# Optimization experiments

Measured on AMD Instinct MI355X. Metric: run time of the kernel, lower is better.

## Reference

```python
import jax, jax.numpy as jnp
import numpy as np

D_MODEL = 1024

def setup_inputs() -> dict:
    key = jax.random.key(0)
    kx, kq, kk, kv, ko = jax.random.split(key, 5)
    x = jax.random.normal(kx, (4, 4096, D_MODEL), dtype=jnp.float32)
    w_q = jax.random.normal(kq, (D_MODEL, D_MODEL), dtype=jnp.float32)
    w_k = jax.random.normal(kk, (D_MODEL, D_MODEL), dtype=jnp.float32)
    w_v = jax.random.normal(kv, (D_MODEL, D_MODEL), dtype=jnp.float32)
    w_o = jax.random.normal(ko, (D_MODEL, D_MODEL), dtype=jnp.float32)
    return {"x": x, "w_q": w_q, "w_k": w_k, "w_v": w_v, "w_o": w_o}

def reference(x, w_q, w_k, w_v, w_o):
    # Q/K/V projections: [B,T,D] @ [D,D] -> [B,T,D]
    q = jnp.einsum('btd,de->bte', x, w_q)
    k = jnp.einsum('btd,de->bte', x, w_k)
    v = jnp.einsum('btd,de->bte', x, w_v)
    # Unnormalized attention: scores [B,T,T] (no softmax)
    scores = jnp.einsum('btd,bsd->bts', q, k)
    attn_output = jnp.einsum('bts,bsd->btd', scores, v)
    # Output projection
    output = jnp.einsum('btd,de->bte', attn_output, w_o)
    return output
```

## Files before the change

kernel.cpp:

```cpp
#include <hip/hip_runtime.h>
#include <hip/hip_bf16.h>
#include <stdint.h>

typedef unsigned short u16;
typedef short bf16x8 __attribute__((ext_vector_type(8)));
typedef float f32x4 __attribute__((ext_vector_type(4)));

#define GLOAD16(gp, lp) __builtin_amdgcn_global_load_lds( \
    (const __attribute__((address_space(1))) uint32_t*)(gp), \
    (__attribute__((address_space(3))) uint32_t*)(lp), 16, 0, 0)

#define VMCNT10 do { asm volatile("s_waitcnt vmcnt(10)" ::: "memory"); \
                     __builtin_amdgcn_sched_barrier(0); } while (0)
#define SBAR    do { __builtin_amdgcn_s_barrier(); \
                     __builtin_amdgcn_sched_barrier(0); } while (0)
#define LGKM0   do { asm volatile("s_waitcnt lgkmcnt(0)" ::: "memory"); \
                     __builtin_amdgcn_sched_barrier(0); } while (0)

__device__ __forceinline__ u16 f2bf(float f) {
  union { float f; uint32_t u; } x; x.f = f;
  return (u16)((x.u + 0x7FFFu + ((x.u >> 16) & 1u)) >> 16);
}
__device__ __forceinline__ float bf2f(u16 h) {
  union { uint32_t u; float f; } x; x.u = (uint32_t)h << 16;
  return x.f;
}

__device__ __forceinline__ void xcd_swizzle(int& bx, int& by, int& bz) {
  const int gx = gridDim.x, gy = gridDim.y;
  const int nwg = gx * gy * (int)gridDim.z;
  const int lin = ((int)blockIdx.z * gy + (int)blockIdx.y) * gx + (int)blockIdx.x;
  const int q = nwg >> 3;
  const int wl = (lin & 7) * q + (lin >> 3);
  bz = wl / (gx * gy);
  const int rem = wl - bz * gx * gy;
  by = rem / gx;
  bx = rem - by * gx;
}

__global__ __launch_bounds__(256) void cast_all(const float* __restrict__ x,
                                                const float* __restrict__ wq,
                                                const float* __restrict__ wk,
                                                const float* __restrict__ wv,
                                                const float* __restrict__ wo,
                                                u16* __restrict__ xb,
                                                u16* __restrict__ xT,
                                                u16* __restrict__ WA,
                                                u16* __restrict__ WBb) {
  __shared__ float tile[64][65];
  const int lin = blockIdx.x;
  const int t = threadIdx.x;
  const int lr = t >> 2, lc = (t & 3) * 16;
  if (lin < 4096) {
    const int d0 = (lin & 15) * 64;
    const int t0 = (lin >> 4) * 64;
    const float* src = x + (size_t)(t0 + lr) * 1024 + d0 + lc;
    u16 pl[16];
#pragma unroll
    for (int j = 0; j < 4; ++j) {
      float4 v = *(const float4*)&src[j * 4];
      tile[lr][lc + j * 4 + 0] = v.x;
      tile[lr][lc + j * 4 + 1] = v.y;
      tile[lr][lc + j * 4 + 2] = v.z;
      tile[lr][lc + j * 4 + 3] = v.w;
      pl[j * 4 + 0] = f2bf(v.x); pl[j * 4 + 1] = f2bf(v.y);
      pl[j * 4 + 2] = f2bf(v.z); pl[j * 4 + 3] = f2bf(v.w);
    }
    u16* pdst = xb + (size_t)(t0 + lr) * 1024 + d0 + lc;
    *(uint4*)&pdst[0] = *(const uint4*)&pl[0];
    *(uint4*)&pdst[8] = *(const uint4*)&pl[8];
    __syncthreads();
    u16 tr[16];
#pragma unroll
    for (int j = 0; j < 16; ++j) tr[j] = f2bf(tile[lc + j][lr]);
    u16* tdst = xT + (size_t)(d0 + lr) * 16384 + t0 + lc;
    *(uint4*)&tdst[0] = *(const uint4*)&tr[0];
    *(uint4*)&tdst[8] = *(const uint4*)&tr[8];
  } else {
    const int w = lin - 4096;
    const int z = w >> 8, tl = w & 255;
    const int r0 = (tl >> 4) * 64, c0 = (tl & 15) * 64;
    const float* in = z == 0 ? wq : z == 1 ? wk : z == 2 ? wv : wo;
    u16* o = z == 0 ? WA : z == 1 ? WBb : z == 2 ? WBb + 1048576 : WA + 1048576;
    const float* src = in + (size_t)(r0 + lr) * 1024 + c0 + lc;
    if (z < 3) {
      u16 p[16];
#pragma unroll
      for (int j = 0; j < 4; ++j) {
        float4 v = *(const float4*)&src[j * 4];
        p[j * 4 + 0] = f2bf(v.x); p[j * 4 + 1] = f2bf(v.y);
        p[j * 4 + 2] = f2bf(v.z); p[j * 4 + 3] = f2bf(v.w);
      }
      u16* dst = o + (size_t)(r0 + lr) * 1024 + c0 + lc;
      *(uint4*)&dst[0] = *(const uint4*)&p[0];
      *(uint4*)&dst[8] = *(const uint4*)&p[8];
    } else {
#pragma unroll
      for (int j = 0; j < 4; ++j) {
        float4 v = *(const float4*)&src[j * 4];
        tile[lr][lc + j * 4 + 0] = v.x;
        tile[lr][lc + j * 4 + 1] = v.y;
        tile[lr][lc + j * 4 + 2] = v.z;
        tile[lr][lc + j * 4 + 3] = v.w;
      }
      __syncthreads();
      u16 tr[16];
#pragma unroll
      for (int j = 0; j < 16; ++j) tr[j] = f2bf(tile[lc + j][lr]);
      u16* dst = o + (size_t)(c0 + lr) * 1024 + r0 + lc;
      *(uint4*)&dst[0] = *(const uint4*)&tr[0];
      *(uint4*)&dst[8] = *(const uint4*)&tr[8];
    }
  }
}

__global__ __launch_bounds__(512) void gemm_bt8(const u16* __restrict__ A,
                                                const u16* __restrict__ B,
                                                u16* __restrict__ C,
                                                int lda, int ldb, int ldc, int K,
                                                size_t sA, size_t sB, size_t sC) {
  __shared__ u16 lds[2 * 8192];
  int bx, by, bz;
  xcd_swizzle(bx, by, bz);
  A += (size_t)bz * sA;
  B += (size_t)bz * sB;
  const int t = threadIdx.x;
  const int l = t & 63;
  const int wid = t >> 6;
  const int wr = wid >> 2, wc = wid & 3;
  const int lr16 = l & 15, hi = l >> 4;
  const int mBase = by * 128;
  const int nBase = bx * 128;

  f32x4 acc[4][2];
#pragma unroll
  for (int m = 0; m < 4; ++m)
#pragma unroll
    for (int n = 0; n < 2; ++n) acc[m][n] = (f32x4){0.f, 0.f, 0.f, 0.f};

  for (int kt = 0; kt < K; kt += 64) {
    __syncthreads();
#pragma unroll
    for (int i = 0; i < 2; ++i) {
      int s = i * 512 + t;
      int row = s >> 3, cp = s & 7;
      int clog = cp ^ (row & 7);
      GLOAD16(A + (size_t)(mBase + row) * lda + kt + clog * 8, &lds[s * 8]);
    }
#pragma unroll
    for (int i = 0; i < 2; ++i) {
      int s = i * 512 + t;
      int row = s >> 3, cp = s & 7;
      int clog = cp ^ (row & 7);
      GLOAD16(B + (size_t)(nBase + row) * ldb + kt + clog * 8, &lds[8192 + s * 8]);
    }
    asm volatile("s_waitcnt vmcnt(0)" ::: "memory");
    __syncthreads();
#pragma unroll
    for (int ks = 0; ks < 2; ++ks) {
      bf16x8 af[4], bfr[2];
#pragma unroll
      for (int m = 0; m < 4; ++m) {
        int row = wr * 64 + m * 16 + lr16;
        int p = (ks * 4 + hi) ^ (row & 7);
        af[m] = *(const bf16x8*)&lds[row * 64 + p * 8];
      }
#pragma unroll
      for (int n = 0; n < 2; ++n) {
        int row = wc * 32 + n * 16 + lr16;
        int p = (ks * 4 + hi) ^ (row & 7);
        bfr[n] = *(const bf16x8*)&lds[8192 + row * 64 + p * 8];
      }
#pragma unroll
      for (int m = 0; m < 4; ++m)
#pragma unroll
        for (int n = 0; n < 2; ++n)
          acc[m][n] = __builtin_amdgcn_mfma_f32_16x16x32_bf16(af[m], bfr[n], acc[m][n], 0, 0, 0);
    }
  }

#pragma unroll
  for (int m = 0; m < 4; ++m) {
    int row0 = mBase + wr * 64 + m * 16 + hi * 4;
#pragma unroll
    for (int n = 0; n < 2; ++n) {
      int col = nBase + wc * 32 + n * 16 + lr16;
      f32x4 v = acc[m][n];
      u16* Cb = C + (size_t)bz * sC;
#pragma unroll
      for (int r = 0; r < 4; ++r) Cb[(size_t)(row0 + r) * ldc + col] = f2bf(v[r]);
    }
  }
}

__global__ __launch_bounds__(512) void gram_tri(const u16* __restrict__ xT,
                                                u16* __restrict__ Gp) {
  __shared__ u16 lds[2 * 8192];
  const int lin = blockIdx.x;
  const int wl = (lin & 7) * 72 + (lin >> 3);
  const int z = wl / 36, t5 = wl - z * 36;
  const int b = z >> 2, kc = z & 3;
  int ti = 0;
  while ((ti + 1) * (ti + 2) / 2 <= t5) ++ti;
  const int tj = t5 - ti * (ti + 1) / 2;
  const u16* Ap = xT + (size_t)b * 4096 + (size_t)kc * 1024;
  const int lda = 16384;
  const int mBase = ti * 128, nBase = tj * 128;

  const int t = threadIdx.x;
  const int l = t & 63;
  const int wid = t >> 6;
  const int wr = wid >> 2, wc = wid & 3;
  const int lr16 = l & 15, hi = l >> 4;

  f32x4 acc[4][2];
#pragma unroll
  for (int m = 0; m < 4; ++m)
#pragma unroll
    for (int n = 0; n < 2; ++n) acc[m][n] = (f32x4){0.f, 0.f, 0.f, 0.f};

  for (int kt = 0; kt < 1024; kt += 64) {
    __syncthreads();
#pragma unroll
    for (int i = 0; i < 2; ++i) {
      int s = i * 512 + t;
      int row = s >> 3, cp = s & 7;
      int clog = cp ^ (row & 7);
      GLOAD16(Ap + (size_t)(mBase + row) * lda + kt + clog * 8, &lds[s * 8]);
    }
#pragma unroll
    for (int i = 0; i < 2; ++i) {
      int s = i * 512 + t;
      int row = s >> 3, cp = s & 7;
      int clog = cp ^ (row & 7);
      GLOAD16(Ap + (size_t)(nBase + row) * lda + kt + clog * 8, &lds[8192 + s * 8]);
    }
    asm volatile("s_waitcnt vmcnt(0)" ::: "memory");
    __syncthreads();
#pragma unroll
    for (int ks = 0; ks < 2; ++ks) {
      bf16x8 af[4], bfr[2];
#pragma unroll
      for (int m = 0; m < 4; ++m) {
        int row = wr * 64 + m * 16 + lr16;
        int p = (ks * 4 + hi) ^ (row & 7);
        af[m] = *(const bf16x8*)&lds[row * 64 + p * 8];
      }
#pragma unroll
      for (int n = 0; n < 2; ++n) {
        int row = wc * 32 + n * 16 + lr16;
        int p = (ks * 4 + hi) ^ (row & 7);
        bfr[n] = *(const bf16x8*)&lds[8192 + row * 64 + p * 8];
      }
#pragma unroll
      for (int m = 0; m < 4; ++m)
#pragma unroll
        for (int n = 0; n < 2; ++n)
          acc[m][n] = __builtin_amdgcn_mfma_f32_16x16x32_bf16(af[m], bfr[n], acc[m][n], 0, 0, 0);
    }
  }

  u16* Cb = Gp + ((size_t)z * 36 + t5) * 16384;
#pragma unroll
  for (int m = 0; m < 4; ++m) {
    int row0 = wr * 64 + m * 16 + hi * 4;
#pragma unroll
    for (int n = 0; n < 2; ++n) {
      int col = wc * 32 + n * 16 + lr16;
      f32x4 v = acc[m][n];
#pragma unroll
      for (int r = 0; r < 4; ++r) Cb[(size_t)(row0 + r) * 128 + col] = f2bf(v[r]);
    }
  }
}

__global__ __launch_bounds__(256) void reduce_mirror(const u16* __restrict__ Gp,
                                                     u16* __restrict__ G) {
  __shared__ u16 ldsT[128][136];
  const int t5 = blockIdx.x;
  const int b = blockIdx.y;
  int ti = 0;
  while ((ti + 1) * (ti + 2) / 2 <= t5) ++ti;
  const int tj = t5 - ti * (ti + 1) / 2;
  const int tid = threadIdx.x;
  const int rr = tid >> 4, ccc = (tid & 15) * 8;
  u16* Gb = G + (size_t)b * 1048576;
  const size_t ZS = (size_t)36 * 16384;
  const u16* base = Gp + ((size_t)(b * 4) * 36 + t5) * 16384;
#pragma unroll
  for (int i = 0; i < 8; ++i) {
    int row = i * 16 + rr;
    const u16* p = base + row * 128 + ccc;
    u16 a0[8], a1[8], a2[8], a3[8], o[8];
    *(uint4*)a0 = *(const uint4*)&p[0];
    *(uint4*)a1 = *(const uint4*)&p[ZS];
    *(uint4*)a2 = *(const uint4*)&p[2 * ZS];
    *(uint4*)a3 = *(const uint4*)&p[3 * ZS];
#pragma unroll
    for (int j = 0; j < 8; ++j)
      o[j] = f2bf(bf2f(a0[j]) + bf2f(a1[j]) + bf2f(a2[j]) + bf2f(a3[j]));
    *(uint4*)&Gb[(size_t)(ti * 128 + row) * 1024 + tj * 128 + ccc] = *(const uint4*)o;
    *(uint4*)&ldsT[row][ccc] = *(const uint4*)o;
  }
  if (ti != tj) {
    __syncthreads();
#pragma unroll
    for (int i = 0; i < 8; ++i) {
      int row = i * 16 + rr;
      u16 m8[8];
#pragma unroll
      for (int j = 0; j < 8; ++j) m8[j] = ldsT[ccc + j][row];
      *(uint4*)&Gb[(size_t)(tj * 128 + row) * 1024 + ti * 128 + ccc] = *(const uint4*)m8;
    }
  }
}

template <bool F32OUT>
__device__ __forceinline__ void gemm256_core(const u16* __restrict__ A,
                                             const u16* __restrict__ B,
                                             void* __restrict__ C,
                                             int lda, int ldb, int ldc, int K,
                                             int mBase, int nBase, u16* lds) {
  const int t = threadIdx.x;
  const int l = t & 63;
  const int wid = t >> 6;
  const int wr = wid >> 2;
  const int wc = wid & 3;
  const int lr16 = l & 15, hi = l >> 4;
  const int rl0 = t >> 3;
  const int rl1 = rl0 + 64;
  const int cp  = t & 7;
  const int cs  = cp ^ (rl0 & 7);
  const int NT = K >> 6;

  f32x4 acc[8][4];
#pragma unroll
  for (int m = 0; m < 8; ++m)
#pragma unroll
    for (int n = 0; n < 4; ++n) acc[m][n] = (f32x4){0.f, 0.f, 0.f, 0.f};

  auto stage = [&](const u16* g0, int ld, u16* d) {
    GLOAD16(g0 + (size_t)rl0 * ld + cs * 8, d + rl0 * 64 + cp * 8);
    GLOAD16(g0 + (size_t)rl1 * ld + cs * 8, d + rl1 * 64 + cp * 8);
  };
  stage(A + (size_t)mBase * lda,          lda, lds + 0);
  stage(B + (size_t)nBase * ldb,          ldb, lds + 16384);
  stage(B + (size_t)(nBase + 128) * ldb,  ldb, lds + 24576);
  stage(A + (size_t)(mBase + 128) * lda,  lda, lds + 8192);
  stage(B + (size_t)nBase * ldb + 64,         ldb, lds + 32768 + 16384);
  stage(A + (size_t)mBase * lda + 64,         lda, lds + 32768);
  stage(B + (size_t)(nBase + 128) * ldb + 64, ldb, lds + 32768 + 24576);

  bf16x8 af[4][2], b0[2][2], b1[2][2];

  for (int tt = 0; tt < NT; ++tt) {
    const int cur = tt & 1;
    u16* bufA = lds + cur * 32768;
    u16* bufB = bufA + 16384;
    u16* bufN = lds + ((tt + 1) & 1) * 32768;
    int t1 = tt + 1; if (t1 >= NT) t1 -= NT;
    int t2 = tt + 2; if (t2 >= NT) t2 -= NT;
    const int k1 = t1 * 64, k2 = t2 * 64;

    VMCNT10;
    SBAR;
    stage(A + (size_t)(mBase + 128) * lda + k1, lda, bufN + 8192);
#pragma unroll
    for (int mi = 0; mi < 4; ++mi) {
      int row = wr * 64 + mi * 16 + lr16;
#pragma unroll
      for (int kk = 0; kk < 2; ++kk) {
        int p = (kk * 4 + hi) ^ (row & 7);
        af[mi][kk] = *(const bf16x8*)&bufA[row * 64 + p * 8];
      }
    }
#pragma unroll
    for (int ni = 0; ni < 2; ++ni) {
      int row = wc * 32 + ni * 16 + lr16;
#pragma unroll
      for (int kk = 0; kk < 2; ++kk) {
        int p = (kk * 4 + hi) ^ (row & 7);
        b0[ni][kk] = *(const bf16x8*)&bufB[row * 64 + p * 8];
      }
    }
    LGKM0;
    __builtin_amdgcn_s_setprio(1);
#pragma unroll
    for (int kk = 0; kk < 2; ++kk)
#pragma unroll
      for (int mi = 0; mi < 4; ++mi)
#pragma unroll
        for (int ni = 0; ni < 2; ++ni)
          acc[mi][ni] = __builtin_amdgcn_mfma_f32_16x16x32_bf16(af[mi][kk], b0[ni][kk], acc[mi][ni], 0, 0, 0);
    __builtin_amdgcn_s_setprio(0);

    VMCNT10;
    SBAR;
    stage(B + (size_t)nBase * ldb + k2, ldb, bufB);
#pragma unroll
    for (int ni = 0; ni < 2; ++ni) {
      int row = 128 + wc * 32 + ni * 16 + lr16;
#pragma unroll
      for (int kk = 0; kk < 2; ++kk) {
        int p = (kk * 4 + hi) ^ (row & 7);
        b1[ni][kk] = *(const bf16x8*)&bufB[row * 64 + p * 8];
      }
    }
    LGKM0;
    __builtin_amdgcn_s_setprio(1);
#pragma unroll
    for (int kk = 0; kk < 2; ++kk)
#pragma unroll
      for (int mi = 0; mi < 4; ++mi)
#pragma unroll
        for (int ni = 0; ni < 2; ++ni)
          acc[mi][2 + ni] = __builtin_amdgcn_mfma_f32_16x16x32_bf16(af[mi][kk], b1[ni][kk], acc[mi][2 + ni], 0, 0, 0);
    __builtin_amdgcn_s_setprio(0);

    VMCNT10;
    SBAR;
    stage(A + (size_t)mBase * lda + k2, lda, bufA);
#pragma unroll
    for (int mi = 0; mi < 4; ++mi) {
      int row = 128 + wr * 64 + mi * 16 + lr16;
#pragma unroll
      for (int kk = 0; kk < 2; ++kk) {
        int p = (kk * 4 + hi) ^ (row & 7);
        af[mi][kk] = *(const bf16x8*)&bufA[row * 64 + p * 8];
      }
    }
    LGKM0;
    __builtin_amdgcn_s_setprio(1);
#pragma unroll
    for (int kk = 0; kk < 2; ++kk)
#pragma unroll
      for (int mi = 0; mi < 4; ++mi)
#pragma unroll
        for (int ni = 0; ni < 2; ++ni)
          acc[4 + mi][2 + ni] = __builtin_amdgcn_mfma_f32_16x16x32_bf16(af[mi][kk], b1[ni][kk], acc[4 + mi][2 + ni], 0, 0, 0);
    __builtin_amdgcn_s_setprio(0);

    SBAR;
    stage(B + (size_t)(nBase + 128) * ldb + k2, ldb, bufB + 8192);
    __builtin_amdgcn_s_setprio(1);
#pragma unroll
    for (int kk = 0; kk < 2; ++kk)
#pragma unroll
      for (int mi = 0; mi < 4; ++mi)
#pragma unroll
        for (int ni = 0; ni < 2; ++ni)
          acc[4 + mi][ni] = __builtin_amdgcn_mfma_f32_16x16x32_bf16(af[mi][kk], b0[ni][kk], acc[4 + mi][ni], 0, 0, 0);
    __builtin_amdgcn_s_setprio(0);
  }

#pragma unroll
  for (int m = 0; m < 8; ++m) {
    int row0 = mBase + (m >> 2) * 128 + wr * 64 + (m & 3) * 16 + hi * 4;
#pragma unroll
    for (int n = 0; n < 4; ++n) {
      int col = nBase + (n >> 1) * 128 + wc * 32 + (n & 1) * 16 + lr16;
      f32x4 v = acc[m][n];
      if (F32OUT) {
        float* Cf = (float*)C;
#pragma unroll
        for (int r = 0; r < 4; ++r) Cf[(size_t)(row0 + r) * ldc + col] = v[r];
      } else {
        u16* Cb = (u16*)C;
#pragma unroll
        for (int r = 0; r < 4; ++r) Cb[(size_t)(row0 + r) * ldc + col] = f2bf(v[r]);
      }
    }
  }
}

__global__ __launch_bounds__(512) void gemm256_out(const u16* __restrict__ xb,
                                                   const u16* __restrict__ PT,
                                                   float* __restrict__ out) {
  __shared__ u16 lds[65536];
  int bx, by, bz;
  xcd_swizzle(bx, by, bz);
  const u16* Bp = PT + (size_t)(by >> 4) * 1048576;
  gemm256_core<true>(xb, Bp, out, 1024, 1024, 1024, 1024, by * 256, bx * 256, lds);
}

extern "C" void kernel_launch(void* const* d_in, const int* in_sizes, int n_in,
                              void* d_out, int out_size, void* d_ws, size_t ws_size,
                              hipStream_t stream) {
  const float* x  = (const float*)d_in[0];
  const float* wq = (const float*)d_in[1];
  const float* wk = (const float*)d_in[2];
  const float* wv = (const float*)d_in[3];
  const float* wo = (const float*)d_in[4];
  float* out = (float*)d_out;

  u16* ws = (u16*)d_ws;
  const size_t MW = 1048576;
  u16* xb  = ws;
  u16* xT  = ws + 16 * MW;
  u16* WA  = ws + 32 * MW;
  u16* WBb = ws + 34 * MW;
  u16* W12 = ws + 36 * MW;
  u16* G   = ws + 38 * MW;
  u16* S   = ws + 42 * MW;
  u16* PT  = ws + 46 * MW;
  u16* Gp  = ws + 50 * MW;

  cast_all<<<5120, 256, 0, stream>>>(x, wq, wk, wv, wo, xb, xT, WA, WBb);

  gemm_bt8<<<dim3(8, 8, 2), 512, 0, stream>>>(WA, WBb, W12,
                                              1024, 1024, 1024, 1024,
                                              MW, MW, MW);
  gram_tri<<<576, 512, 0, stream>>>(xT, Gp);
  reduce_mirror<<<dim3(36, 4), 256, 0, stream>>>(Gp, G);

  gemm_bt8<<<dim3(8, 8, 4), 512, 0, stream>>>(W12 + MW, G, S,
                                              1024, 1024, 1024, 1024,
                                              0, MW, MW);
  gemm_bt8<<<dim3(8, 8, 4), 512, 0, stream>>>(S, W12, PT,
                                              1024, 1024, 1024, 1024,
                                              MW, 0, MW);
  gemm256_out<<<dim3(4, 64), 512, 0, stream>>>(xb, PT, out);
}
```

Before: 164.5 us.

## Merge weight-product GEMM into gram kernel launch and restructure x cast/transpose

Fuses the W12 weight-product GEMM (128 tiles) with the triangular Gram kernel (576 tiles) into one 704-block launch, removing a launch and letting the small GEMM fill idle CUs alongside the Gram work. The x cast kernel now has each block handle 64x256 tiles, transposing already-converted bf16 values in LDS and writing 128-byte contiguous rows of xT instead of 32-byte pieces. This cuts the cast grid from 5120 to 2048 blocks and removes a second f2bf pass. The risk is LDS bank conflicts from the u16 transpose stores and a uniform XCD swizzle across heterogeneous tiles.

```diff
diff --git a/kernel.cpp b/kernel.cpp
--- a/kernel.cpp
+++ b/kernel.cpp
@@ -47,41 +47,45 @@
                                                 u16* __restrict__ xT,
                                                 u16* __restrict__ WA,
                                                 u16* __restrict__ WBb) {
-  __shared__ float tile[64][65];
+  __shared__ u16 ldsT[64][264];
   const int lin = blockIdx.x;
   const int t = threadIdx.x;
-  const int lr = t >> 2, lc = (t & 3) * 16;
-  if (lin < 4096) {
-    const int d0 = (lin & 15) * 64;
-    const int t0 = (lin >> 4) * 64;
-    const float* src = x + (size_t)(t0 + lr) * 1024 + d0 + lc;
-    u16 pl[16];
-#pragma unroll
-    for (int j = 0; j < 4; ++j) {
-      float4 v = *(const float4*)&src[j * 4];
-      tile[lr][lc + j * 4 + 0] = v.x;
-      tile[lr][lc + j * 4 + 1] = v.y;
-      tile[lr][lc + j * 4 + 2] = v.z;
-      tile[lr][lc + j * 4 + 3] = v.w;
-      pl[j * 4 + 0] = f2bf(v.x); pl[j * 4 + 1] = f2bf(v.y);
-      pl[j * 4 + 2] = f2bf(v.z); pl[j * 4 + 3] = f2bf(v.w);
-    }
-    u16* pdst = xb + (size_t)(t0 + lr) * 1024 + d0 + lc;
-    *(uint4*)&pdst[0] = *(const uint4*)&pl[0];
-    *(uint4*)&pdst[8] = *(const uint4*)&pl[8];
+  if (lin < 1024) {
+    const int dt = lin >> 6;
+    const int tt = lin & 63;
+    const int d0 = dt * 64, t0 = tt * 256;
+    const int lr = t >> 2, lc = (t & 3) * 16;
+#pragma unroll
+    for (int i = 0; i < 4; ++i) {
+      const int row = t0 + i * 64 + lr;
+      const float* src = x + (size_t)row * 1024 + d0 + lc;
+      u16 pl[16];
+#pragma unroll
+      for (int j = 0; j < 4; ++j) {
+        float4 v = *(const float4*)&src[j * 4];
+        pl[j * 4 + 0] = f2bf(v.x); pl[j * 4 + 1] = f2bf(v.y);
+        pl[j * 4 + 2] = f2bf(v.z); pl[j * 4 + 3] = f2bf(v.w);
+      }
+      u16* pdst = xb + (size_t)row * 1024 + d0 + lc;
+      *(uint4*)&pdst[0] = *(const uint4*)&pl[0];
+      *(uint4*)&pdst[8] = *(const uint4*)&pl[8];
+#pragma unroll
+      for (int j = 0; j < 16; ++j) ldsT[lc + j][i * 64 + lr] = pl[j];
+    }
     __syncthreads();
-    u16 tr[16];
-#pragma unroll
-    for (int j = 0; j < 16; ++j) tr[j] = f2bf(tile[lc + j][lr]);
-    u16* tdst = xT + (size_t)(d0 + lr) * 16384 + t0 + lc;
-    *(uint4*)&tdst[0] = *(const uint4*)&tr[0];
-    *(uint4*)&tdst[8] = *(const uint4*)&tr[8];
+    const int dl = t >> 2, seg = (t & 3) * 64;
+    u16* dst = xT + (size_t)(d0 + dl) * 16384 + t0 + seg;
+    const u16* srcl = &ldsT[dl][seg];
+#pragma unroll
+    for (int k = 0; k < 8; ++k)
+      *(uint4*)&dst[k * 8] = *(const uint4*)&srcl[k * 8];
   } else {
-    const int w = lin - 4096;
+    const int w = lin - 1024;
     const int z = w >> 8, tl = w & 255;
     const int r0 = (tl >> 4) * 64, c0 = (tl & 15) * 64;
     const float* in = z == 0 ? wq : z == 1 ? wk : z == 2 ? wv : wo;
     u16* o = z == 0 ? WA : z == 1 ? WBb : z == 2 ? WBb + 1048576 : WA + 1048576;
+    const int lr = t >> 2, lc = (t & 3) * 16;
     const float* src = in + (size_t)(r0 + lr) * 1024 + c0 + lc;
     if (z < 3) {
       u16 p[16];
@@ -95,6 +99,7 @@
       *(uint4*)&dst[0] = *(const uint4*)&p[0];
       *(uint4*)&dst[8] = *(const uint4*)&p[8];
     } else {
+      float (*tile)[65] = (float(*)[65])ldsT;
 #pragma unroll
       for (int j = 0; j < 4; ++j) {
         float4 v = *(const float4*)&src[j * 4];
@@ -110,6 +115,106 @@
       u16* dst = o + (size_t)(c0 + lr) * 1024 + r0 + lc;
       *(uint4*)&dst[0] = *(const uint4*)&tr[0];
       *(uint4*)&dst[8] = *(const uint4*)&tr[8];
+    }
+  }
+}
+
+__global__ __launch_bounds__(512) void gram_w12(const u16* __restrict__ xT,
+                                                u16* __restrict__ Gp,
+                                                const u16* __restrict__ WA,
+                                                const u16* __restrict__ WBb,
+                                                u16* __restrict__ W12) {
+  __shared__ u16 lds[2 * 8192];
+  const int lin = blockIdx.x;
+  const int wl = (lin & 7) * 88 + (lin >> 3);
+  const u16 *A, *B;
+  u16* Cb;
+  int lda, ldc;
+  if (wl < 576) {
+    const int z = wl / 36, t5 = wl - z * 36;
+    const int b = z >> 2, kc = z & 3;
+    int ti = 0;
+    while ((ti + 1) * (ti + 2) / 2 <= t5) ++ti;
+    const int tj = t5 - ti * (ti + 1) / 2;
+    const u16* Ap = xT + (size_t)b * 4096 + (size_t)kc * 1024;
+    A = Ap + (size_t)(ti * 128) * 16384;
+    B = Ap + (size_t)(tj * 128) * 16384;
+    lda = 16384;
+    Cb = Gp + ((size_t)z * 36 + t5) * 16384;
+    ldc = 128;
+  } else {
+    const int w = wl - 576;
+    const int z2 = w >> 6, tl = w & 63;
+    const int by = tl >> 3, bx = tl & 7;
+    A = WA + (size_t)z2 * 1048576 + (size_t)(by * 128) * 1024;
+    B = WBb + (size_t)z2 * 1048576 + (size_t)(bx * 128) * 1024;
+    lda = 1024;
+    Cb = W12 + (size_t)z2 * 1048576 + (size_t)(by * 128) * 1024 + bx * 128;
+    ldc = 1024;
+  }
+
+  const int t = threadIdx.x;
+  const int l = t & 63;
+  const int wid = t >> 6;
+  const int wr = wid >> 2, wc = wid & 3;
+  const int lr16 = l & 15, hi = l >> 4;
+
+  f32x4 acc[4][2];
+#pragma unroll
+  for (int m = 0; m < 4; ++m)
+#pragma unroll
+    for (int n = 0; n < 2; ++n) acc[m][n] = (f32x4){0.f, 0.f, 0.f, 0.f};
+
+  for (int kt = 0; kt < 1024; kt += 64) {
+    __syncthreads();
+#pragma unroll
+    for (int i = 0; i < 2; ++i) {
+      int s = i * 512 + t;
+      int row = s >> 3, cp = s & 7;
+      int clog = cp ^ (row & 7);
+      GLOAD16(A + (size_t)row * lda + kt + clog * 8, &lds[s * 8]);
+    }
+#pragma unroll
+    for (int i = 0; i < 2; ++i) {
+      int s = i * 512 + t;
+      int row = s >> 3, cp = s & 7;
+      int clog = cp ^ (row & 7);
+      GLOAD16(B + (size_t)row * lda + kt + clog * 8, &lds[8192 + s * 8]);
+    }
+    asm volatile("s_waitcnt vmcnt(0)" ::: "memory");
+    __syncthreads();
+#pragma unroll
+    for (int ks = 0; ks < 2; ++ks) {
+      bf16x8 af[4], bfr[2];
+#pragma unroll
+      for (int m = 0; m < 4; ++m) {
+        int row = wr * 64 + m * 16 + lr16;
+        int p = (ks * 4 + hi) ^ (row & 7);
+        af[m] = *(const bf16x8*)&lds[row * 64 + p * 8];
+      }
+#pragma unroll
+      for (int n = 0; n < 2; ++n) {
+        int row = wc * 32 + n * 16 + lr16;
+        int p = (ks * 4 + hi) ^ (row & 7);
+        bfr[n] = *(const bf16x8*)&lds[8192 + row * 64 + p * 8];
+      }
+#pragma unroll
+      for (int m = 0; m < 4; ++m)
+#pragma unroll
+        for (int n = 0; n < 2; ++n)
+          acc[m][n] = __builtin_amdgcn_mfma_f32_16x16x32_bf16(af[m], bfr[n], acc[m][n], 0, 0, 0);
+    }
+  }
+
+#pragma unroll
+  for (int m = 0; m < 4; ++m) {
+    int row0 = wr * 64 + m * 16 + hi * 4;
+#pragma unroll
+    for (int n = 0; n < 2; ++n) {
+      int col = wc * 32 + n * 16 + lr16;
+      f32x4 v = acc[m][n];
+#pragma unroll
+      for (int r = 0; r < 4; ++r) Cb[(size_t)(row0 + r) * ldc + col] = f2bf(v[r]);
     }
   }
 }
@@ -193,87 +298,6 @@
   }
 }
 
-__global__ __launch_bounds__(512) void gram_tri(const u16* __restrict__ xT,
-                                                u16* __restrict__ Gp) {
-  __shared__ u16 lds[2 * 8192];
-  const int lin = blockIdx.x;
-  const int wl = (lin & 7) * 72 + (lin >> 3);
-  const int z = wl / 36, t5 = wl - z * 36;
-  const int b = z >> 2, kc = z & 3;
-  int ti = 0;
-  while ((ti + 1) * (ti + 2) / 2 <= t5) ++ti;
-  const int tj = t5 - ti * (ti + 1) / 2;
-  const u16* Ap = xT + (size_t)b * 4096 + (size_t)kc * 1024;
-  const int lda = 16384;
-  const int mBase = ti * 128, nBase = tj * 128;
-
-  const int t = threadIdx.x;
-  const int l = t & 63;
-  const int wid = t >> 6;
-  const int wr = wid >> 2, wc = wid & 3;
-  const int lr16 = l & 15, hi = l >> 4;
-
-  f32x4 acc[4][2];
-#pragma unroll
-  for (int m = 0; m < 4; ++m)
-#pragma unroll
-    for (int n = 0; n < 2; ++n) acc[m][n] = (f32x4){0.f, 0.f, 0.f, 0.f};
-
-  for (int kt = 0; kt < 1024; kt += 64) {
-    __syncthreads();
-#pragma unroll
-    for (int i = 0; i < 2; ++i) {
-      int s = i * 512 + t;
-      int row = s >> 3, cp = s & 7;
-      int clog = cp ^ (row & 7);
-      GLOAD16(Ap + (size_t)(mBase + row) * lda + kt + clog * 8, &lds[s * 8]);
-    }
-#pragma unroll
-    for (int i = 0; i < 2; ++i) {
-      int s = i * 512 + t;
-      int row = s >> 3, cp = s & 7;
-      int clog = cp ^ (row & 7);
-      GLOAD16(Ap + (size_t)(nBase + row) * lda + kt + clog * 8, &lds[8192 + s * 8]);
-    }
-    asm volatile("s_waitcnt vmcnt(0)" ::: "memory");
-    __syncthreads();
-#pragma unroll
-    for (int ks = 0; ks < 2; ++ks) {
-      bf16x8 af[4], bfr[2];
-#pragma unroll
-      for (int m = 0; m < 4; ++m) {
-        int row = wr * 64 + m * 16 + lr16;
-        int p = (ks * 4 + hi) ^ (row & 7);
-        af[m] = *(const bf16x8*)&lds[row * 64 + p * 8];
-      }
-#pragma unroll
-      for (int n = 0; n < 2; ++n) {
-        int row = wc * 32 + n * 16 + lr16;
-        int p = (ks * 4 + hi) ^ (row & 7);
-        bfr[n] = *(const bf16x8*)&lds[8192 + row * 64 + p * 8];
-      }
-#pragma unroll
-      for (int m = 0; m < 4; ++m)
-#pragma unroll
-        for (int n = 0; n < 2; ++n)
-          acc[m][n] = __builtin_amdgcn_mfma_f32_16x16x32_bf16(af[m], bfr[n], acc[m][n], 0, 0, 0);
-    }
-  }
-
-  u16* Cb = Gp + ((size_t)z * 36 + t5) * 16384;
-#pragma unroll
-  for (int m = 0; m < 4; ++m) {
-    int row0 = wr * 64 + m * 16 + hi * 4;
-#pragma unroll
-    for (int n = 0; n < 2; ++n) {
-      int col = wc * 32 + n * 16 + lr16;
-      f32x4 v = acc[m][n];
-#pragma unroll
-      for (int r = 0; r < 4; ++r) Cb[(size_t)(row0 + r) * 128 + col] = f2bf(v[r]);
-    }
-  }
-}
-
 __global__ __launch_bounds__(256) void reduce_mirror(const u16* __restrict__ Gp,
                                                      u16* __restrict__ G) {
   __shared__ u16 ldsT[128][136];
@@ -505,12 +529,9 @@
   u16* PT  = ws + 46 * MW;
   u16* Gp  = ws + 50 * MW;
 
-  cast_all<<<5120, 256, 0, stream>>>(x, wq, wk, wv, wo, xb, xT, WA, WBb);
-
-  gemm_bt8<<<dim3(8, 8, 2), 512, 0, stream>>>(WA, WBb, W12,
-                                              1024, 1024, 1024, 1024,
-                                              MW, MW, MW);
-  gram_tri<<<576, 512, 0, stream>>>(xT, Gp);
+  cast_all<<<2048, 256, 0, stream>>>(x, wq, wk, wv, wo, xb, xT, WA, WBb);
+
+  gram_w12<<<704, 512, 0, stream>>>(xT, Gp, WA, WBb, W12);
   reduce_mirror<<<dim3(36, 4), 256, 0, stream>>>(Gp, G);
 
   gemm_bt8<<<dim3(8, 8, 4), 512, 0, stream>>>(W12 + MW, G, S,
```

Result: faster. 156.2 us (-5.1%).
